# Optimization experiments

Measured on AMD Instinct MI355X. Metric: run time of the kernel, lower is better.

Reference implementation:

```python
import jax, jax.numpy as jnp
import numpy as np

NUM_HEADS = 16
LN_EPS = 1e-05


def setup_inputs() -> dict:
    key = jax.random.key(0)
    ks = jax.random.split(key, 10)
    B, S, H = 2, 2048, 1024
    s = 1.0 / np.sqrt(H)
    return {
        "hidden_states": jax.random.normal(ks[0], (B, S, H), dtype=jnp.float32),
        "Wq": jax.random.normal(ks[1], (H, H), dtype=jnp.float32) * s,
        "bq": jax.random.normal(ks[2], (H,), dtype=jnp.float32) * 0.02,
        "Wk": jax.random.normal(ks[3], (H, H), dtype=jnp.float32) * s,
        "bk": jax.random.normal(ks[4], (H,), dtype=jnp.float32) * 0.02,
        "Wv": jax.random.normal(ks[5], (H, H), dtype=jnp.float32) * s,
        "bv": jax.random.normal(ks[6], (H,), dtype=jnp.float32) * 0.02,
        "Wd": jax.random.normal(ks[7], (H, H), dtype=jnp.float32) * s,
        "bd": jax.random.normal(ks[8], (H,), dtype=jnp.float32) * 0.02,
        "ln_gamma": jnp.ones((H,), dtype=jnp.float32),
        "ln_beta": jnp.zeros((H,), dtype=jnp.float32),
    }


def reference(hidden_states, Wq, bq, Wk, bk, Wv, bv, Wd, bd, ln_gamma, ln_beta):
    B, S, H = hidden_states.shape
    nh = NUM_HEADS
    hd = H // nh

    # QKV projections (torch Linear: x @ W.T + b), split heads -> [B, nh, S, hd]
    def proj(W, b):
        y = jnp.einsum('bsh,oh->bso', hidden_states, W) + b
        return y.reshape(B, S, nh, hd).transpose(0, 2, 1, 3)

    q = proj(Wq, bq)
    k = proj(Wk, bk)
    v = proj(Wv, bv)

    # scaled dot-product attention: [B, nh, S, S]
    scores = jnp.einsum('bhqd,bhkd->bhqk', q, k) / jnp.sqrt(jnp.float32(hd))
    probs = jax.nn.softmax(scores, axis=-1)
    ctx = jnp.einsum('bhqk,bhkd->bhqd', probs, v)  # [B, nh, S, hd]
    ctx = ctx.transpose(0, 2, 1, 3).reshape(B, S, H)

    # output dense + residual + LayerNorm
    attn_out = jnp.einsum('bsh,oh->bso', ctx, Wd) + bd
    x = attn_out + hidden_states
    mu = jnp.mean(x, axis=-1, keepdims=True)
    var = jnp.mean(jnp.square(x - mu), axis=-1, keepdims=True)
    return (x - mu) * jax.lax.rsqrt(var + LN_EPS) * ln_gamma + ln_beta
```

## Files before the change

kernel.cpp:

```cpp
#include <hip/hip_runtime.h>

constexpr int kH    = 1024;
constexpr int kSEQ  = 2048;
constexpr int kBATCH= 2;
constexpr int kNH   = 16;
constexpr int kHD   = 64;
constexpr int kM    = 4096;
constexpr int kSPLIT= 4;
constexpr int kKEYS = kSEQ / kSPLIT;

typedef _Float16 h8  __attribute__((ext_vector_type(8)));
typedef _Float16 h4  __attribute__((ext_vector_type(4)));
typedef float   f32x4  __attribute__((ext_vector_type(4)));
typedef float   f32x16 __attribute__((ext_vector_type(16)));

static __device__ __forceinline__ f32x4 mfma16(h8 a, h8 b, f32x4 c) {
  return __builtin_amdgcn_mfma_f32_16x16x32_f16(a, b, c, 0, 0, 0);
}
static __device__ __forceinline__ f32x16 mfma32(h8 a, h8 b, f32x16 c) {
  return __builtin_amdgcn_mfma_f32_32x32x16_f16(a, b, c, 0, 0, 0);
}

static __device__ __forceinline__ void gll16(const _Float16* g, _Float16* l) {
  __builtin_amdgcn_global_load_lds(
      (const __attribute__((address_space(1))) void*)g,
      (__attribute__((address_space(3))) void*)l, 16, 0, 0);
}

#define QSCALE 0.18033688011112042f
#define C0INIT (-5.770780163555854f)

__global__ __launch_bounds__(256) void cvt_all(
    const float* __restrict__ X,  const float* __restrict__ Wq,
    const float* __restrict__ Wk, const float* __restrict__ Wv,
    const float* __restrict__ Wd,
    _Float16* __restrict__ Xh,  _Float16* __restrict__ Wqh,
    _Float16* __restrict__ Wkh, _Float16* __restrict__ Wvh,
    _Float16* __restrict__ Wdh)
{
  int i = blockIdx.x * 256 + threadIdx.x;
  const float* src; _Float16* dst; int off;
  if (i < (kM * kH) / 4) {
    src = X; dst = Xh; off = i;
  } else {
    int j = i - (kM * kH) / 4;
    int w = j >> 18;
    off = j & 262143;
    src = (w == 0) ? Wq : (w == 1) ? Wk : (w == 2) ? Wv : Wd;
    dst = (w == 0) ? Wqh : (w == 1) ? Wkh : (w == 2) ? Wvh : Wdh;
  }
  float4 v = reinterpret_cast<const float4*>(src)[off];
  h4 o;
  o[0] = (_Float16)v.x; o[1] = (_Float16)v.y;
  o[2] = (_Float16)v.z; o[3] = (_Float16)v.w;
  reinterpret_cast<h4*>(dst)[off] = o;
}

__global__ __launch_bounds__(256, 2) void qkv_gemm(
    const _Float16* __restrict__ Xh,
    const _Float16* __restrict__ Wq, const _Float16* __restrict__ Wk,
    const _Float16* __restrict__ Wv,
    const float* __restrict__ bq, const float* __restrict__ bk,
    const float* __restrict__ bv,
    _Float16* __restrict__ Qo, _Float16* __restrict__ Ko, _Float16* __restrict__ Vo)
{
  const int proj = blockIdx.z;
  const _Float16* W   = (proj == 0) ? Wq : ((proj == 1) ? Wk : Wv);
  const float*    bias= (proj == 0) ? bq : ((proj == 1) ? bk : bv);
  _Float16*       Out = (proj == 0) ? Qo : ((proj == 1) ? Ko : Vo);

  const int m0 = blockIdx.y * 128, n0 = blockIdx.x * 128;
  __shared__ __align__(16) _Float16 As[2][128 * 32];
  __shared__ __align__(16) _Float16 Bs[2][128 * 32];

  const int tid  = threadIdx.x;
  const int wave = tid >> 6, lane = tid & 63, quad = lane >> 4, l16 = lane & 15;
  const int mw = (wave & 1) * 64, nw = (wave >> 1) * 64;

  f32x4 acc[4][4] = {};
  const int grow = wave * 32 + (lane >> 2);
  const int gcol = (lane & 3) * 8;
  const _Float16* Ag = Xh + (size_t)(m0 + grow) * kH + gcol;
  const _Float16* Bg = W  + (size_t)(n0 + grow) * kH + gcol;

  {
    gll16(Ag,            &As[0][wave * 1024]);
    gll16(Ag + 16 * kH,  &As[0][wave * 1024 + 512]);
    gll16(Bg,            &Bs[0][wave * 1024]);
    gll16(Bg + 16 * kH,  &Bs[0][wave * 1024 + 512]);
  }

  for (int k = 0; k < 32; ++k) {
    const int cur = k & 1;
    __syncthreads();
    if (k < 31) {
      const int k0 = (k + 1) * 32, nb = cur ^ 1;
      gll16(Ag + k0,           &As[nb][wave * 1024]);
      gll16(Ag + 16 * kH + k0, &As[nb][wave * 1024 + 512]);
      gll16(Bg + k0,           &Bs[nb][wave * 1024]);
      gll16(Bg + 16 * kH + k0, &Bs[nb][wave * 1024 + 512]);
    }
    h8 af[4], bf[4];
    #pragma unroll
    for (int mi = 0; mi < 4; ++mi)
      af[mi] = *reinterpret_cast<const h8*>(&As[cur][(mw + mi * 16 + l16) * 32 + quad * 8]);
    #pragma unroll
    for (int ni = 0; ni < 4; ++ni)
      bf[ni] = *reinterpret_cast<const h8*>(&Bs[cur][(nw + ni * 16 + l16) * 32 + quad * 8]);
    #pragma unroll
    for (int mi = 0; mi < 4; ++mi)
      #pragma unroll
      for (int ni = 0; ni < 4; ++ni)
        acc[mi][ni] = mfma16(af[mi], bf[ni], acc[mi][ni]);
  }

  __syncthreads();
  _Float16* Crows = (mw == 0) ? &As[0][0] : &Bs[0][0];
  #pragma unroll
  for (int mi = 0; mi < 4; ++mi)
  #pragma unroll
  for (int ni = 0; ni < 4; ++ni) {
    const int col = nw + ni * 16 + l16;
    const float bv_ = bias[n0 + col];
    #pragma unroll
    for (int r = 0; r < 4; ++r) {
      const int rr = mi * 16 + quad * 4 + r;
      float val = acc[mi][ni][r] + bv_;
      if (proj == 0) val *= QSCALE;
      const int chunk = (col >> 3) ^ (rr & 7);
      Crows[rr * 128 + chunk * 8 + (col & 7)] = (_Float16)val;
    }
  }
  __syncthreads();
  {
    const int r = tid >> 1;
    const int halfc = tid & 1;
    const _Float16* base = (r < 64) ? &As[0][0] : &Bs[0][0];
    const int rr = r & 63;
    const int mg = m0 + r;
    const int bb = mg >> 11, srow = mg & 2047;
    const int ng0 = n0 + halfc * 64;
    const int hh = ng0 >> 6;
    _Float16* dst = Out + (((size_t)(bb * kNH + hh) * kSEQ) + srow) * kHD;
    #pragma unroll
    for (int c8 = 0; c8 < 8; ++c8) {
      const int col0 = halfc * 64 + c8 * 8;
      const int chunk = (col0 >> 3) ^ (rr & 7);
      h8 v = *reinterpret_cast<const h8*>(&base[rr * 128 + chunk * 8]);
      *reinterpret_cast<h8*>(dst + c8 * 8) = v;
    }
  }
}

__global__ __launch_bounds__(256) void vtrans(const _Float16* __restrict__ V,
                                              _Float16* __restrict__ Vt)
{
  const int st = blockIdx.x;
  const int bh = blockIdx.y;
  __shared__ __align__(16) _Float16 Lt[64][72];
  const int t = threadIdx.x, r = t >> 2, c = (t & 3) * 16;
  const _Float16* src = V + (size_t)bh * kSEQ * kHD + (size_t)(st * 64 + r) * kHD + c;
  h8 p0 = *reinterpret_cast<const h8*>(src);
  h8 p1 = *reinterpret_cast<const h8*>(src + 8);
  #pragma unroll
  for (int e = 0; e < 8; ++e) Lt[c + e][r] = p0[e];
  #pragma unroll
  for (int e = 0; e < 8; ++e) Lt[c + 8 + e][r] = p1[e];
  __syncthreads();
  _Float16* dst = Vt + (size_t)bh * kHD * kSEQ + (size_t)r * kSEQ + st * 64 + c;
  *reinterpret_cast<h8*>(dst)     = *reinterpret_cast<const h8*>(&Lt[r][c]);
  *reinterpret_cast<h8*>(dst + 8) = *reinterpret_cast<const h8*>(&Lt[r][c + 8]);
}

__global__ __launch_bounds__(256, 2) void attn_kernel(
    const _Float16* __restrict__ Q, const _Float16* __restrict__ K,
    const _Float16* __restrict__ Vt, _Float16* __restrict__ Op,
    float* __restrict__ lp)
{
  const int qt = blockIdx.x, bh = blockIdx.y, split = blockIdx.z;
  const int tid = threadIdx.x;
  const int wave = tid >> 6, lane = tid & 63;
  const int quad = lane >> 4, l16 = lane & 15;
  const int lane32 = lane & 31, half = lane >> 5;

  __shared__ __align__(16) _Float16 Kl[2][64 * 64];
  __shared__ __align__(16) _Float16 Vl[2][64 * 64];
  __shared__ __align__(16) _Float16 Pl[4][32 * 64];

  const _Float16* Qb = Q  + (size_t)bh * kSEQ * kHD;
  const _Float16* Kb = K  + (size_t)bh * kSEQ * kHD;
  const _Float16* Vb = Vt + (size_t)bh * kHD * kSEQ;
  const int soff = split * kKEYS;
  const int qbase = qt * 256 + wave * 64;

  h8 qf[2][4];
  #pragma unroll
  for (int qc = 0; qc < 2; ++qc)
    #pragma unroll
    for (int kt = 0; kt < 4; ++kt)
      qf[qc][kt] = *reinterpret_cast<const h8*>(
          &Qb[(size_t)(qbase + qc * 32 + lane32) * kHD + kt * 16 + half * 8]);

  const int srow = lane >> 3;
  const int sch  = (lane & 7) ^ srow;
  const _Float16* Kg = Kb + (size_t)(soff + wave * 16 + srow) * kHD + sch * 8;
  const _Float16* Vg = Vb + (size_t)(wave * 16 + srow) * kSEQ + soff + sch * 8;

  f32x4 o[4][4] = {};
  float l_acc[2] = {0.f, 0.f};
  f32x16 cinit;
  #pragma unroll
  for (int r = 0; r < 16; ++r) cinit[r] = C0INIT;

  #pragma unroll
  for (int i = 0; i < 2; ++i) {
    gll16(Kg + (size_t)i * 8 * kHD,     &Kl[0][(wave * 16 + i * 8) * 64]);
    gll16(Vg + (size_t)i * 8 * kSEQ,    &Vl[0][(wave * 16 + i * 8) * 64]);
  }

  for (int kt = 0; kt < kKEYS / 64; ++kt) {
    const int cur = kt & 1;
    __syncthreads();
    if (kt + 1 < kKEYS / 64) {
      const int nb = cur ^ 1;
      const int ko = (kt + 1) * 64;
      #pragma unroll
      for (int i = 0; i < 2; ++i) {
        gll16(Kg + (size_t)(ko + i * 8) * kHD,      &Kl[nb][(wave * 16 + i * 8) * 64]);
        gll16(Vg + (size_t)i * 8 * kSEQ + ko,       &Vl[nb][(wave * 16 + i * 8) * 64]);
      }
    }
    const _Float16* Kc = Kl[cur];
    const _Float16* Vc = Vl[cur];
    _Float16* PlW = Pl[wave];

    h8 ka[2][4];
    #pragma unroll
    for (int kc = 0; kc < 2; ++kc)
      #pragma unroll
      for (int dt = 0; dt < 4; ++dt)
        ka[kc][dt] = *reinterpret_cast<const h8*>(
            &Kc[(kc * 32 + lane32) * 64 + (((dt * 2 + half) ^ (lane32 & 7)) * 8)]);
    h8 vbf[4][2];
    #pragma unroll
    for (int dt = 0; dt < 4; ++dt)
      #pragma unroll
      for (int kc = 0; kc < 2; ++kc)
        vbf[dt][kc] = *reinterpret_cast<const h8*>(
            &Vc[(dt * 16 + l16) * 64 + (((kc * 4 + quad) ^ (l16 & 7)) * 8)]);

    #pragma unroll
    for (int qc = 0; qc < 2; ++qc) {
      f32x16 s0 = cinit, s1 = cinit;
      #pragma unroll
      for (int dt = 0; dt < 4; ++dt) s0 = mfma32(ka[0][dt], qf[qc][dt], s0);
      #pragma unroll
      for (int dt = 0; dt < 4; ++dt) s1 = mfma32(ka[1][dt], qf[qc][dt], s1);

      float la = 0.f;
      #pragma unroll
      for (int kc = 0; kc < 2; ++kc) {
        const f32x16& sv = kc ? s1 : s0;
        #pragma unroll
        for (int g = 0; g < 4; ++g) {
          float e0 = exp2f(sv[4 * g + 0]);
          float e1 = exp2f(sv[4 * g + 1]);
          float e2 = exp2f(sv[4 * g + 2]);
          float e3 = exp2f(sv[4 * g + 3]);
          la += (e0 + e1) + (e2 + e3);
          h4 pp;
          pp[0] = (_Float16)e0; pp[1] = (_Float16)e1;
          pp[2] = (_Float16)e2; pp[3] = (_Float16)e3;
          *reinterpret_cast<h4*>(
              &PlW[lane32 * 64 + (((kc * 4 + g) ^ (lane32 & 7)) * 8) + half * 4]) = pp;
        }
      }
      l_acc[qc] += la;

      h8 pa[2][2];
      #pragma unroll
      for (int qh = 0; qh < 2; ++qh)
        #pragma unroll
        for (int kc = 0; kc < 2; ++kc)
          pa[qh][kc] = *reinterpret_cast<const h8*>(
              &PlW[(qh * 16 + l16) * 64 + (((kc * 4 + quad) ^ (l16 & 7)) * 8)]);
      #pragma unroll
      for (int qh = 0; qh < 2; ++qh)
        #pragma unroll
        for (int dt = 0; dt < 4; ++dt) {
          o[qc * 2 + qh][dt] = mfma16(pa[qh][0], vbf[dt][0], o[qc * 2 + qh][dt]);
          o[qc * 2 + qh][dt] = mfma16(pa[qh][1], vbf[dt][1], o[qc * 2 + qh][dt]);
        }
    }
  }

  const size_t pbase = ((size_t)(split * (kBATCH * kNH) + bh)) * kSEQ;
  #pragma unroll
  for (int qc = 0; qc < 2; ++qc) {
    l_acc[qc] += __shfl_xor(l_acc[qc], 32);
    if (half == 0) lp[pbase + qbase + qc * 32 + lane32] = l_acc[qc];
  }
  #pragma unroll
  for (int qh = 0; qh < 4; ++qh)
    #pragma unroll
    for (int r = 0; r < 4; ++r) {
      const int q = qbase + qh * 16 + quad * 4 + r;
      #pragma unroll
      for (int dt = 0; dt < 4; ++dt)
        Op[(pbase + q) * kHD + dt * 16 + l16] = (_Float16)o[qh][dt][r];
    }
}

__global__ __launch_bounds__(256) void attn_merge(
    const _Float16* __restrict__ Op, const float* __restrict__ lp,
    _Float16* __restrict__ Ctx)
{
  const int t = blockIdx.x * 256 + threadIdx.x;
  const int d8 = t & 7, q = (t >> 3) & (kSEQ - 1), bh = t >> 14;
  float acc[8] = {};
  float l = 0.f;
  #pragma unroll
  for (int s = 0; s < kSPLIT; ++s) {
    const size_t pbase = ((size_t)(s * (kBATCH * kNH) + bh)) * kSEQ + q;
    h8 v = *reinterpret_cast<const h8*>(&Op[pbase * kHD + d8 * 8]);
    #pragma unroll
    for (int e = 0; e < 8; ++e) acc[e] += (float)v[e];
    l += lp[pbase];
  }
  const float inv = 1.f / l;
  const int b = bh >> 4, hh = bh & 15;
  h8 ov;
  #pragma unroll
  for (int e = 0; e < 8; ++e) ov[e] = (_Float16)(acc[e] * inv);
  *reinterpret_cast<h8*>(&Ctx[((size_t)(b * kSEQ + q)) * kH + hh * kHD + d8 * 8]) = ov;
}

__global__ __launch_bounds__(256, 2) void dense_gemm(
    const _Float16* __restrict__ A, const _Float16* __restrict__ W,
    const float* __restrict__ bias, const float* __restrict__ resid,
    float* __restrict__ Out)
{
  const int m0 = blockIdx.y * 128, n0 = blockIdx.x * 128;
  __shared__ __align__(16) _Float16 As[2][128 * 32];
  __shared__ __align__(16) _Float16 Bs[2][128 * 32];
  const int tid  = threadIdx.x;
  const int wave = tid >> 6, lane = tid & 63, quad = lane >> 4, l16 = lane & 15;
  const int mw = (wave & 1) * 64, nw = (wave >> 1) * 64;
  f32x4 acc[4][4] = {};
  const int grow = wave * 32 + (lane >> 2);
  const int gcol = (lane & 3) * 8;
  const _Float16* Ag = A + (size_t)(m0 + grow) * kH + gcol;
  const _Float16* Bg = W + (size_t)(n0 + grow) * kH + gcol;

  {
    gll16(Ag,           &As[0][wave * 1024]);
    gll16(Ag + 16 * kH, &As[0][wave * 1024 + 512]);
    gll16(Bg,           &Bs[0][wave * 1024]);
    gll16(Bg + 16 * kH, &Bs[0][wave * 1024 + 512]);
  }

  for (int k = 0; k < 32; ++k) {
    const int cur = k & 1;
    __syncthreads();
    if (k < 31) {
      const int k0 = (k + 1) * 32, nb = cur ^ 1;
      gll16(Ag + k0,           &As[nb][wave * 1024]);
      gll16(Ag + 16 * kH + k0, &As[nb][wave * 1024 + 512]);
      gll16(Bg + k0,           &Bs[nb][wave * 1024]);
      gll16(Bg + 16 * kH + k0, &Bs[nb][wave * 1024 + 512]);
    }
    h8 af[4], bf[4];
    #pragma unroll
    for (int mi = 0; mi < 4; ++mi)
      af[mi] = *reinterpret_cast<const h8*>(&As[cur][(mw + mi * 16 + l16) * 32 + quad * 8]);
    #pragma unroll
    for (int ni = 0; ni < 4; ++ni)
      bf[ni] = *reinterpret_cast<const h8*>(&Bs[cur][(nw + ni * 16 + l16) * 32 + quad * 8]);
    #pragma unroll
    for (int mi = 0; mi < 4; ++mi)
      #pragma unroll
      for (int ni = 0; ni < 4; ++ni)
        acc[mi][ni] = mfma16(af[mi], bf[ni], acc[mi][ni]);
  }
  #pragma unroll
  for (int mi = 0; mi < 4; ++mi)
  #pragma unroll
  for (int ni = 0; ni < 4; ++ni) {
    const int ng = n0 + nw + ni * 16 + l16;
    const float bv_ = bias[ng];
    #pragma unroll
    for (int r = 0; r < 4; ++r) {
      const int mg = m0 + mw + mi * 16 + quad * 4 + r;
      Out[(size_t)mg * kH + ng] = acc[mi][ni][r] + bv_ + resid[(size_t)mg * kH + ng];
    }
  }
}

__global__ __launch_bounds__(256) void ln_kernel(const float* __restrict__ Tmp,
    const float* __restrict__ gamma, const float* __restrict__ beta,
    float* __restrict__ out)
{
  const int row = blockIdx.x;
  const float4 v = reinterpret_cast<const float4*>(Tmp + (size_t)row * kH)[threadIdx.x];
  float s  = v.x + v.y + v.z + v.w;
  float ss = v.x * v.x + v.y * v.y + v.z * v.z + v.w * v.w;
  #pragma unroll
  for (int off = 32; off > 0; off >>= 1) {
    s  += __shfl_down(s, off);
    ss += __shfl_down(ss, off);
  }
  __shared__ float red[8];
  const int wave = threadIdx.x >> 6, lane = threadIdx.x & 63;
  if (lane == 0) { red[wave] = s; red[4 + wave] = ss; }
  __syncthreads();
  s  = red[0] + red[1] + red[2] + red[3];
  ss = red[4] + red[5] + red[6] + red[7];
  const float mu   = s * (1.f / kH);
  const float var  = ss * (1.f / kH) - mu * mu;
  const float rstd = rsqrtf(var + 1e-5f);
  const float4 g  = reinterpret_cast<const float4*>(gamma)[threadIdx.x];
  const float4 bb = reinterpret_cast<const float4*>(beta)[threadIdx.x];
  float4 o;
  o.x = (v.x - mu) * rstd * g.x + bb.x;
  o.y = (v.y - mu) * rstd * g.y + bb.y;
  o.z = (v.z - mu) * rstd * g.z + bb.z;
  o.w = (v.w - mu) * rstd * g.w + bb.w;
  reinterpret_cast<float4*>(out + (size_t)row * kH)[threadIdx.x] = o;
}

extern "C" void kernel_launch(void* const* d_in, const int* in_sizes, int n_in,
                              void* d_out, int out_size, void* d_ws, size_t ws_size,
                              hipStream_t stream) {
  const float* hs    = (const float*)d_in[0];
  const float* Wq    = (const float*)d_in[1];
  const float* bq    = (const float*)d_in[2];
  const float* Wk    = (const float*)d_in[3];
  const float* bk    = (const float*)d_in[4];
  const float* Wv    = (const float*)d_in[5];
  const float* bv    = (const float*)d_in[6];
  const float* Wd    = (const float*)d_in[7];
  const float* bd    = (const float*)d_in[8];
  const float* gamma = (const float*)d_in[9];
  const float* beta  = (const float*)d_in[10];
  float* out = (float*)d_out;

  char* ws = (char*)d_ws;
  _Float16* Xh   = (_Float16*)(ws + 0);
  _Float16* Wqh  = (_Float16*)(ws + 8388608);
  _Float16* Wkh  = (_Float16*)(ws + 10485760);
  _Float16* Wvh  = (_Float16*)(ws + 12582912);
  _Float16* Wdh  = (_Float16*)(ws + 14680064);
  _Float16* Qh   = (_Float16*)(ws + 16777216);
  _Float16* Kh   = (_Float16*)(ws + 25165824);
  _Float16* Vh   = (_Float16*)(ws + 33554432);
  _Float16* Vtb  = Xh;
  float*    lpart= (float*)Wqh;
  _Float16* Opart= (_Float16*)(ws + 33554432);
  _Float16* Ctx  = Qh;
  float*    Tmp  = (float*)(ws + 50331648);

  cvt_all<<<8192, 256, 0, stream>>>(hs, Wq, Wk, Wv, Wd, Xh, Wqh, Wkh, Wvh, Wdh);
  qkv_gemm<<<dim3(kH / 128, kM / 128, 3), 256, 0, stream>>>(
      Xh, Wqh, Wkh, Wvh, bq, bk, bv, Qh, Kh, Vh);
  vtrans<<<dim3(kSEQ / 64, kBATCH * kNH), 256, 0, stream>>>(Vh, Vtb);
  attn_kernel<<<dim3(kSEQ / 256, kBATCH * kNH, kSPLIT), 256, 0, stream>>>(
      Qh, Kh, Vtb, Opart, lpart);
  attn_merge<<<2048, 256, 0, stream>>>(Opart, lpart, Ctx);
  dense_gemm<<<dim3(kH / 128, kM / 128), 256, 0, stream>>>(Ctx, Wdh, bd, hs, Tmp);
  ln_kernel<<<kM, 256, 0, stream>>>(Tmp, gamma, beta, out);
}
```

Baseline: 238.7 us.

## Keep attention P in registers and load K/V directly without LDS

The attention kernel drops LDS staging of K, V and P. K and V fragments are loaded from global memory straight into registers with register double-buffering over 32-key steps. The probability tile is rebuilt into the PV MFMA operand layout with a cross-half lane shuffle instead of an LDS round trip, and PV now uses 32x32 MFMAs with a transposed (d-major) partial output. The merge kernel is rewritten to read that transposed layout and transpose it back through shared memory. This removes barriers and LDS traffic, at the cost of each wave re-reading K/V from global or L2 without block-level sharing, and higher register pressure.

```diff
diff --git a/kernel.cpp b/kernel.cpp
--- a/kernel.cpp
+++ b/kernel.cpp
@@ -11,6 +11,7 @@
 
 typedef _Float16 h8  __attribute__((ext_vector_type(8)));
 typedef _Float16 h4  __attribute__((ext_vector_type(4)));
+typedef float   f32x2  __attribute__((ext_vector_type(2)));
 typedef float   f32x4  __attribute__((ext_vector_type(4)));
 typedef float   f32x16 __attribute__((ext_vector_type(16)));
 
@@ -180,159 +181,169 @@
   const int qt = blockIdx.x, bh = blockIdx.y, split = blockIdx.z;
   const int tid = threadIdx.x;
   const int wave = tid >> 6, lane = tid & 63;
-  const int quad = lane >> 4, l16 = lane & 15;
-  const int lane32 = lane & 31, half = lane >> 5;
-
-  __shared__ __align__(16) _Float16 Kl[2][64 * 64];
-  __shared__ __align__(16) _Float16 Vl[2][64 * 64];
-  __shared__ __align__(16) _Float16 Pl[4][32 * 64];
+  const int lane32 = lane & 31;
+  const bool hi = (lane >> 5) != 0;
 
   const _Float16* Qb = Q  + (size_t)bh * kSEQ * kHD;
   const _Float16* Kb = K  + (size_t)bh * kSEQ * kHD;
   const _Float16* Vb = Vt + (size_t)bh * kHD * kSEQ;
   const int soff = split * kKEYS;
   const int qbase = qt * 256 + wave * 64;
+  const int h8off = (lane >> 5) * 8;
 
   h8 qf[2][4];
   #pragma unroll
   for (int qc = 0; qc < 2; ++qc)
     #pragma unroll
-    for (int kt = 0; kt < 4; ++kt)
-      qf[qc][kt] = *reinterpret_cast<const h8*>(
-          &Qb[(size_t)(qbase + qc * 32 + lane32) * kHD + kt * 16 + half * 8]);
-
-  const int srow = lane >> 3;
-  const int sch  = (lane & 7) ^ srow;
-  const _Float16* Kg = Kb + (size_t)(soff + wave * 16 + srow) * kHD + sch * 8;
-  const _Float16* Vg = Vb + (size_t)(wave * 16 + srow) * kSEQ + soff + sch * 8;
-
-  f32x4 o[4][4] = {};
+    for (int dt = 0; dt < 4; ++dt)
+      qf[qc][dt] = *reinterpret_cast<const h8*>(
+          &Qb[(size_t)(qbase + qc * 32 + lane32) * kHD + dt * 16 + h8off]);
+
+  const _Float16* Kg = Kb + (size_t)(soff + lane32) * kHD + h8off;
+  const _Float16* Vg = Vb + (size_t)lane32 * kSEQ + soff + h8off;
+
+  h8 ka0[4], ka1[4];
+  h8 va0[2][2], va1[2][2];
+
+  #pragma unroll
+  for (int dt = 0; dt < 4; ++dt)
+    ka0[dt] = *reinterpret_cast<const h8*>(Kg + dt * 16);
+  #pragma unroll
+  for (int mt = 0; mt < 2; ++mt)
+    #pragma unroll
+    for (int kc = 0; kc < 2; ++kc)
+      va0[mt][kc] = *reinterpret_cast<const h8*>(Vg + (size_t)mt * 32 * kSEQ + kc * 16);
+
+  f32x16 o[2][2] = {};
   float l_acc[2] = {0.f, 0.f};
   f32x16 cinit;
   #pragma unroll
   for (int r = 0; r < 16; ++r) cinit[r] = C0INIT;
 
-  #pragma unroll
-  for (int i = 0; i < 2; ++i) {
-    gll16(Kg + (size_t)i * 8 * kHD,     &Kl[0][(wave * 16 + i * 8) * 64]);
-    gll16(Vg + (size_t)i * 8 * kSEQ,    &Vl[0][(wave * 16 + i * 8) * 64]);
-  }
-
-  for (int kt = 0; kt < kKEYS / 64; ++kt) {
-    const int cur = kt & 1;
-    __syncthreads();
-    if (kt + 1 < kKEYS / 64) {
-      const int nb = cur ^ 1;
-      const int ko = (kt + 1) * 64;
-      #pragma unroll
-      for (int i = 0; i < 2; ++i) {
-        gll16(Kg + (size_t)(ko + i * 8) * kHD,      &Kl[nb][(wave * 16 + i * 8) * 64]);
-        gll16(Vg + (size_t)i * 8 * kSEQ + ko,       &Vl[nb][(wave * 16 + i * 8) * 64]);
-      }
-    }
-    const _Float16* Kc = Kl[cur];
-    const _Float16* Vc = Vl[cur];
-    _Float16* PlW = Pl[wave];
-
-    h8 ka[2][4];
-    #pragma unroll
-    for (int kc = 0; kc < 2; ++kc)
+  constexpr int NIT = kKEYS / 32;
+
+  auto step = [&](const h8 (&kaC)[4], const h8 (&vaC)[2][2],
+                  h8 (&kaN)[4], h8 (&vaN)[2][2], int kt) {
+    if (kt + 1 < NIT) {
+      const int ko = (kt + 1) * 32;
       #pragma unroll
       for (int dt = 0; dt < 4; ++dt)
-        ka[kc][dt] = *reinterpret_cast<const h8*>(
-            &Kc[(kc * 32 + lane32) * 64 + (((dt * 2 + half) ^ (lane32 & 7)) * 8)]);
-    h8 vbf[4][2];
-    #pragma unroll
-    for (int dt = 0; dt < 4; ++dt)
-      #pragma unroll
-      for (int kc = 0; kc < 2; ++kc)
-        vbf[dt][kc] = *reinterpret_cast<const h8*>(
-            &Vc[(dt * 16 + l16) * 64 + (((kc * 4 + quad) ^ (l16 & 7)) * 8)]);
-
+        kaN[dt] = *reinterpret_cast<const h8*>(Kg + (size_t)ko * kHD + dt * 16);
+      #pragma unroll
+      for (int mt = 0; mt < 2; ++mt)
+        #pragma unroll
+        for (int kc = 0; kc < 2; ++kc)
+          vaN[mt][kc] = *reinterpret_cast<const h8*>(
+              Vg + (size_t)mt * 32 * kSEQ + ko + kc * 16);
+    }
     #pragma unroll
     for (int qc = 0; qc < 2; ++qc) {
-      f32x16 s0 = cinit, s1 = cinit;
-      #pragma unroll
-      for (int dt = 0; dt < 4; ++dt) s0 = mfma32(ka[0][dt], qf[qc][dt], s0);
-      #pragma unroll
-      for (int dt = 0; dt < 4; ++dt) s1 = mfma32(ka[1][dt], qf[qc][dt], s1);
-
+      f32x16 s = cinit;
+      #pragma unroll
+      for (int dt = 0; dt < 4; ++dt) s = mfma32(kaC[dt], qf[qc][dt], s);
       float la = 0.f;
       #pragma unroll
       for (int kc = 0; kc < 2; ++kc) {
-        const f32x16& sv = kc ? s1 : s0;
-        #pragma unroll
-        for (int g = 0; g < 4; ++g) {
-          float e0 = exp2f(sv[4 * g + 0]);
-          float e1 = exp2f(sv[4 * g + 1]);
-          float e2 = exp2f(sv[4 * g + 2]);
-          float e3 = exp2f(sv[4 * g + 3]);
-          la += (e0 + e1) + (e2 + e3);
-          h4 pp;
-          pp[0] = (_Float16)e0; pp[1] = (_Float16)e1;
-          pp[2] = (_Float16)e2; pp[3] = (_Float16)e3;
-          *reinterpret_cast<h4*>(
-              &PlW[lane32 * 64 + (((kc * 4 + g) ^ (lane32 & 7)) * 8) + half * 4]) = pp;
-        }
+        float a0 = exp2f(s[kc * 8 + 0]), a1 = exp2f(s[kc * 8 + 1]);
+        float a2 = exp2f(s[kc * 8 + 2]), a3 = exp2f(s[kc * 8 + 3]);
+        float b0 = exp2f(s[kc * 8 + 4]), b1 = exp2f(s[kc * 8 + 5]);
+        float b2 = exp2f(s[kc * 8 + 6]), b3 = exp2f(s[kc * 8 + 7]);
+        la += ((a0 + a1) + (a2 + a3)) + ((b0 + b1) + (b2 + b3));
+        h4 pA, pB;
+        pA[0] = (_Float16)a0; pA[1] = (_Float16)a1;
+        pA[2] = (_Float16)a2; pA[3] = (_Float16)a3;
+        pB[0] = (_Float16)b0; pB[1] = (_Float16)b1;
+        pB[2] = (_Float16)b2; pB[3] = (_Float16)b3;
+        h4 psend = hi ? pA : pB;
+        f32x2 t = __builtin_bit_cast(f32x2, psend);
+        f32x2 rsh;
+        rsh[0] = __shfl_xor(t[0], 32);
+        rsh[1] = __shfl_xor(t[1], 32);
+        h4 pr = __builtin_bit_cast(h4, rsh);
+        h4 lo4 = hi ? pr : pA;
+        h4 hi4 = hi ? pB : pr;
+        h8 pb;
+        pb[0] = lo4[0]; pb[1] = lo4[1]; pb[2] = lo4[2]; pb[3] = lo4[3];
+        pb[4] = hi4[0]; pb[5] = hi4[1]; pb[6] = hi4[2]; pb[7] = hi4[3];
+        o[qc][0] = mfma32(vaC[0][kc], pb, o[qc][0]);
+        o[qc][1] = mfma32(vaC[1][kc], pb, o[qc][1]);
       }
       l_acc[qc] += la;
-
-      h8 pa[2][2];
-      #pragma unroll
-      for (int qh = 0; qh < 2; ++qh)
-        #pragma unroll
-        for (int kc = 0; kc < 2; ++kc)
-          pa[qh][kc] = *reinterpret_cast<const h8*>(
-              &PlW[(qh * 16 + l16) * 64 + (((kc * 4 + quad) ^ (l16 & 7)) * 8)]);
-      #pragma unroll
-      for (int qh = 0; qh < 2; ++qh)
-        #pragma unroll
-        for (int dt = 0; dt < 4; ++dt) {
-          o[qc * 2 + qh][dt] = mfma16(pa[qh][0], vbf[dt][0], o[qc * 2 + qh][dt]);
-          o[qc * 2 + qh][dt] = mfma16(pa[qh][1], vbf[dt][1], o[qc * 2 + qh][dt]);
-        }
-    }
-  }
-
-  const size_t pbase = ((size_t)(split * (kBATCH * kNH) + bh)) * kSEQ;
+    }
+  };
+
+  for (int kt = 0; kt < NIT; kt += 2) {
+    step(ka0, va0, ka1, va1, kt);
+    step(ka1, va1, ka0, va0, kt + 1);
+  }
+
+  const size_t obase = (size_t)(split * (kBATCH * kNH) + bh) * kHD * kSEQ;
+  const size_t lbase = (size_t)(split * (kBATCH * kNH) + bh) * kSEQ;
   #pragma unroll
   for (int qc = 0; qc < 2; ++qc) {
-    l_acc[qc] += __shfl_xor(l_acc[qc], 32);
-    if (half == 0) lp[pbase + qbase + qc * 32 + lane32] = l_acc[qc];
-  }
-  #pragma unroll
-  for (int qh = 0; qh < 4; ++qh)
-    #pragma unroll
-    for (int r = 0; r < 4; ++r) {
-      const int q = qbase + qh * 16 + quad * 4 + r;
-      #pragma unroll
-      for (int dt = 0; dt < 4; ++dt)
-        Op[(pbase + q) * kHD + dt * 16 + l16] = (_Float16)o[qh][dt][r];
-    }
+    float lt = l_acc[qc] + __shfl_xor(l_acc[qc], 32);
+    if (!hi) lp[lbase + qbase + qc * 32 + lane32] = lt;
+    const int qg = qbase + qc * 32 + lane32;
+    #pragma unroll
+    for (int mt = 0; mt < 2; ++mt)
+      #pragma unroll
+      for (int r = 0; r < 16; ++r) {
+        const int d = mt * 32 + (r & 3) + 8 * (r >> 2) + (hi ? 4 : 0);
+        Op[obase + (size_t)d * kSEQ + qg] = (_Float16)o[qc][mt][r];
+      }
+  }
 }
 
 __global__ __launch_bounds__(256) void attn_merge(
     const _Float16* __restrict__ Op, const float* __restrict__ lp,
     _Float16* __restrict__ Ctx)
 {
-  const int t = blockIdx.x * 256 + threadIdx.x;
-  const int d8 = t & 7, q = (t >> 3) & (kSEQ - 1), bh = t >> 14;
-  float acc[8] = {};
-  float l = 0.f;
-  #pragma unroll
-  for (int s = 0; s < kSPLIT; ++s) {
-    const size_t pbase = ((size_t)(s * (kBATCH * kNH) + bh)) * kSEQ + q;
-    h8 v = *reinterpret_cast<const h8*>(&Op[pbase * kHD + d8 * 8]);
-    #pragma unroll
-    for (int e = 0; e < 8; ++e) acc[e] += (float)v[e];
-    l += lp[pbase];
-  }
-  const float inv = 1.f / l;
-  const int b = bh >> 4, hh = bh & 15;
-  h8 ov;
-  #pragma unroll
-  for (int e = 0; e < 8; ++e) ov[e] = (_Float16)(acc[e] * inv);
-  *reinterpret_cast<h8*>(&Ctx[((size_t)(b * kSEQ + q)) * kH + hh * kHD + d8 * 8]) = ov;
+  const int qt = blockIdx.x;
+  const int bh = blockIdx.y;
+  __shared__ float linv[64];
+  __shared__ __align__(16) _Float16 Ls[64][72];
+  const int tid = threadIdx.x;
+
+  if (tid < 64) {
+    float l = 0.f;
+    #pragma unroll
+    for (int s = 0; s < kSPLIT; ++s)
+      l += lp[(size_t)(s * (kBATCH * kNH) + bh) * kSEQ + qt * 64 + tid];
+    linv[tid] = 1.f / l;
+  }
+
+  {
+    const int d = tid >> 2, q0 = (tid & 3) * 16;
+    float acc[16] = {};
+    #pragma unroll
+    for (int s = 0; s < kSPLIT; ++s) {
+      const size_t base = ((size_t)(s * (kBATCH * kNH) + bh) * kHD + d) * kSEQ
+                          + qt * 64 + q0;
+      h8 v0 = *reinterpret_cast<const h8*>(Op + base);
+      h8 v1 = *reinterpret_cast<const h8*>(Op + base + 8);
+      #pragma unroll
+      for (int e = 0; e < 8; ++e) { acc[e] += (float)v0[e]; acc[8 + e] += (float)v1[e]; }
+    }
+    #pragma unroll
+    for (int e = 0; e < 16; ++e) Ls[q0 + e][d] = (_Float16)acc[e];
+  }
+  __syncthreads();
+  {
+    const int q = tid >> 2, dc = (tid & 3) * 16;
+    const float inv = linv[q];
+    const int b = bh >> 4, hh = bh & 15;
+    h8 v0 = *reinterpret_cast<const h8*>(&Ls[q][dc]);
+    h8 v1 = *reinterpret_cast<const h8*>(&Ls[q][dc + 8]);
+    h8 o0, o1;
+    #pragma unroll
+    for (int e = 0; e < 8; ++e) {
+      o0[e] = (_Float16)((float)v0[e] * inv);
+      o1[e] = (_Float16)((float)v1[e] * inv);
+    }
+    _Float16* dst = Ctx + ((size_t)(b * kSEQ + qt * 64 + q)) * kH + hh * kHD + dc;
+    *reinterpret_cast<h8*>(dst)     = o0;
+    *reinterpret_cast<h8*>(dst + 8) = o1;
+  }
 }
 
 __global__ __launch_bounds__(256, 2) void dense_gemm(
@@ -465,7 +476,7 @@
   vtrans<<<dim3(kSEQ / 64, kBATCH * kNH), 256, 0, stream>>>(Vh, Vtb);
   attn_kernel<<<dim3(kSEQ / 256, kBATCH * kNH, kSPLIT), 256, 0, stream>>>(
       Qh, Kh, Vtb, Opart, lpart);
-  attn_merge<<<2048, 256, 0, stream>>>(Opart, lpart, Ctx);
+  attn_merge<<<dim3(kSEQ / 64, kBATCH * kNH), 256, 0, stream>>>(Opart, lpart, Ctx);
   dense_gemm<<<dim3(kH / 128, kM / 128), 256, 0, stream>>>(Ctx, Wdh, bd, hs, Tmp);
   ln_kernel<<<kM, 256, 0, stream>>>(Tmp, gamma, beta, out);
 }
```

Measured after the change: 274.5 us. 15.0% more time.
